# Optimization experiments

Hardware: AMD Instinct MI355X
Metric: run time of the kernel (lower is better)

The kernel has to match this reference:

```python
import jax, jax.numpy as jnp
import numpy as np
from jax import lax

SCALE = 0.05  # keep gates out of saturation

def _lstm_layer(x, w_ih, w_hh, b_ih, b_hh):
    # x: [B, T, In]; w_ih: [4H, In]; w_hh: [4H, H]; PyTorch gate order i,f,g,o
    B = x.shape[0]
    H = w_hh.shape[1]
    # precompute input contribution for all timesteps: [B, T, 4H]
    xg = jnp.einsum('bti,gi->btg', x, w_ih) + b_ih + b_hh
    h0 = jnp.zeros((B, H), dtype=x.dtype)
    c0 = jnp.zeros((B, H), dtype=x.dtype)

    def step(carry, xg_t):
        h, c = carry
        gates = xg_t + h @ w_hh.T  # [B, 4H]
        i, f, g, o = jnp.split(gates, 4, axis=-1)
        i = jax.nn.sigmoid(i)
        f = jax.nn.sigmoid(f)
        g = jnp.tanh(g)
        o = jax.nn.sigmoid(o)
        c = f * c + i * g
        h = o * jnp.tanh(c)
        return (h, c), h

    (h_T, c_T), hs = lax.scan(step, (h0, c0), xg.transpose(1, 0, 2))  # hs: [T, B, H]
    return hs.transpose(1, 0, 2), h_T, c_T


def setup_inputs() -> dict:
    key = jax.random.key(0)
    ks = jax.random.split(key, 12)
    B, T, In, H = 128, 1024, 128, 256
    G = 4 * H
    inp = {
        'x': jax.random.normal(ks[0], (B, T, In), dtype=jnp.float32),
        'w_ih_l0': jax.random.normal(ks[1], (G, In), dtype=jnp.float32) * SCALE,
        'w_hh_l0': jax.random.normal(ks[2], (G, H), dtype=jnp.float32) * SCALE,
        'b_ih_l0': jax.random.normal(ks[3], (G,), dtype=jnp.float32) * SCALE,
        'b_hh_l0': jax.random.normal(ks[4], (G,), dtype=jnp.float32) * SCALE,
        'w_ih_l1': jax.random.normal(ks[5], (G, H), dtype=jnp.float32) * SCALE,
        'w_hh_l1': jax.random.normal(ks[6], (G, H), dtype=jnp.float32) * SCALE,
        'b_ih_l1': jax.random.normal(ks[7], (G,), dtype=jnp.float32) * SCALE,
        'b_hh_l1': jax.random.normal(ks[8], (G,), dtype=jnp.float32) * SCALE,
        'w_lin': jax.random.normal(ks[9], (In, H), dtype=jnp.float32) * SCALE,
        'b_lin': jax.random.normal(ks[10], (In,), dtype=jnp.float32) * SCALE,
    }
    return inp


def reference(x, w_ih_l0, w_hh_l0, b_ih_l0, b_hh_l0,
              w_ih_l1, w_hh_l1, b_ih_l1, b_hh_l1, w_lin, b_lin):
    h0_seq, h0, c0 = _lstm_layer(x, w_ih_l0, w_hh_l0, b_ih_l0, b_hh_l0)
    h1_seq, h1, c1 = _lstm_layer(h0_seq, w_ih_l1, w_hh_l1, b_ih_l1, b_hh_l1)
    out = jnp.einsum('bth,oh->bto', h1_seq, w_lin) + b_lin  # [B, T, In]
    h = jnp.stack([h0, h1], axis=0)  # [num_layers, B, H]
    c = jnp.stack([c0, c1], axis=0)
    return out, (h, c)
```

## Files before the change

### kernel.cpp

```cpp
#include <hip/hip_runtime.h>
#include <hip/hip_bf16.h>

typedef __attribute__((ext_vector_type(8))) short short8;
typedef __attribute__((ext_vector_type(4))) float floatx4;
typedef __attribute__((ext_vector_type(4))) unsigned int uint4v;
typedef __attribute__((ext_vector_type(2))) _Float16 f16x2;

#define B_ 128
#define T_ 1024
#define H_ 256
#define G_ 1024

#if defined(__has_builtin)
#  if __has_builtin(__builtin_amdgcn_fdot2)
#    define HAS_FDOT2 1
#  endif
#endif

__device__ __forceinline__ float sigmoidf_(float x) {
    return 1.0f / (1.0f + __expf(-x));
}
__device__ __forceinline__ float tanhf_(float x) {
    float e = __expf(2.0f * x);
    return 1.0f - 2.0f / (e + 1.0f);
}
__device__ __forceinline__ unsigned short f2bu(float x) {
    __hip_bfloat16 b = __float2bfloat16(x);
    return *reinterpret_cast<unsigned short*>(&b);
}

__device__ __forceinline__ float dot2_(unsigned int w, unsigned int h, float acc) {
#ifdef HAS_FDOT2
    return __builtin_amdgcn_fdot2(__builtin_bit_cast(f16x2, w),
                                  __builtin_bit_cast(f16x2, h), acc, false);
#else
    float d;
    asm("v_dot2_f32_f16 %0, %1, %2, %3" : "=v"(d) : "v"(w), "v"(h), "v"(acc));
    return d;
#endif
}

struct GParam {
    const float* A;
    const float* Wt;
    const float* bias1;
    const float* bias2;
    float* C;
    int d2shift;
    long sa1, sa2, sc1, sc2;
    int K;
    int valid;
};

__global__ __launch_bounds__(256) void gemm_bias_f32(GParam P)
{
    __shared__ __hip_bfloat16 a_tile[64][40];
    __shared__ __hip_bfloat16 b_tile[64][40];

    const int tid  = threadIdx.x;
    const int wave = tid >> 6;
    const int lane = tid & 63;
    const int quad = lane >> 4;
    const int l16  = lane & 15;

    const int bm = blockIdx.x * 64;
    const int bn = blockIdx.y * 64;
    const int mask = (1 << P.d2shift) - 1;

    const int lr  = tid >> 2;
    const int seg = tid & 3;

    const int grow = bm + lr;
    const float* abase =
        P.A + (long)(grow >> P.d2shift) * P.sa1 + (long)(grow & mask) * P.sa2 + seg * 8;
    const float* bbase = P.Wt + (long)(bn + lr) * P.K + seg * 8;

    floatx4 acc[4];
    #pragma unroll
    for (int nt = 0; nt < 4; ++nt) acc[nt] = (floatx4){0.f, 0.f, 0.f, 0.f};

    for (int kk = 0; kk < P.K; kk += 32) {
        float4 a0 = *(const float4*)(abase + kk);
        float4 a1 = *(const float4*)(abase + kk + 4);
        float4 b0 = *(const float4*)(bbase + kk);
        float4 b1 = *(const float4*)(bbase + kk + 4);
        uint4 ap, bp;
        ap.x = f2bu(a0.x) | ((unsigned)f2bu(a0.y) << 16);
        ap.y = f2bu(a0.z) | ((unsigned)f2bu(a0.w) << 16);
        ap.z = f2bu(a1.x) | ((unsigned)f2bu(a1.y) << 16);
        ap.w = f2bu(a1.z) | ((unsigned)f2bu(a1.w) << 16);
        bp.x = f2bu(b0.x) | ((unsigned)f2bu(b0.y) << 16);
        bp.y = f2bu(b0.z) | ((unsigned)f2bu(b0.w) << 16);
        bp.z = f2bu(b1.x) | ((unsigned)f2bu(b1.y) << 16);
        bp.w = f2bu(b1.z) | ((unsigned)f2bu(b1.w) << 16);
        __syncthreads();
        *(uint4*)&a_tile[lr][seg * 8] = ap;
        *(uint4*)&b_tile[lr][seg * 8] = bp;
        __syncthreads();
        short8 af = *(const short8*)&a_tile[wave * 16 + l16][quad * 8];
        #pragma unroll
        for (int nt = 0; nt < 4; ++nt) {
            short8 bf = *(const short8*)&b_tile[nt * 16 + l16][quad * 8];
            acc[nt] = __builtin_amdgcn_mfma_f32_16x16x32_bf16(af, bf, acc[nt], 0, 0, 0);
        }
    }

    #pragma unroll
    for (int nt = 0; nt < 4; ++nt) {
        const int col = bn + nt * 16 + l16;
        float bsum = P.bias1[col];
        if (P.bias2) bsum += P.bias2[col];
        #pragma unroll
        for (int r = 0; r < 4; ++r) {
            const int rm = bm + wave * 16 + quad * 4 + r;
            const long off = (long)(rm >> P.d2shift) * P.sc1 + (long)(rm & mask) * P.sc2;
            P.C[off + col] = acc[nt][r] + bsum;
        }
    }
}

__global__ __launch_bounds__(256) void pack_whh(
    const float* __restrict__ w,
    unsigned int* __restrict__ wrg,
    unsigned int* __restrict__ wo)
{
    const int idx = blockIdx.x * 256 + threadIdx.x;
    if (idx < 98304) {
        const int kh = idx / 49152;
        const int r  = idx % 49152;
        const int g  = r >> 14;
        const int r2 = r & 16383;
        const int kp = r2 >> 8;
        const int jj = r2 & 255;
        const long src = (long)(g * 256 + jj) * 256 + kh * 128 + kp * 2;
        f16x2 pk;
        pk.x = (_Float16)w[src];
        pk.y = (_Float16)w[src + 1];
        wrg[idx] = __builtin_bit_cast(unsigned int, pk);
    } else {
        const int i2 = idx - 98304;
        const int jj = i2 >> 7;
        const int kp = i2 & 127;
        const long src = (long)(768 + jj) * 256 + kp * 2;
        f16x2 pk;
        pk.x = (_Float16)w[src];
        pk.y = (_Float16)w[src + 1];
        wo[i2] = __builtin_bit_cast(unsigned int, pk);
    }
}

struct LArgs {
    const float* xg;
    const unsigned int* wrg;
    const unsigned int* wo;
    float* h_seq;
    const float* h_in;
    const float* c_in;
    float* h_out;
    float* c_out;
    float* c_fin;
    int Tc;
    int init;
    int valid;
};

__device__ __forceinline__ void lstm_body(const LArgs& A, int b)
{
    const int tid = threadIdx.x;
    const int j   = tid & 255;
    const int kh  = tid >> 8;

    __shared__ __align__(16) unsigned int wo_lds[32768];
    __shared__ __align__(16) float part[256][4];
    __shared__ __align__(16) _Float16 hpk[256];

    const int Tc = A.Tc;

    unsigned int wi_[64], wf_[64], wg_[64];
    {
        const unsigned int* wb = A.wrg + (long)kh * 49152 + j;
        #pragma unroll
        for (int kp = 0; kp < 64; ++kp) wi_[kp] = wb[kp * 256];
        #pragma unroll
        for (int kp = 0; kp < 64; ++kp) wf_[kp] = wb[16384 + kp * 256];
        #pragma unroll
        for (int kp = 0; kp < 64; ++kp) wg_[kp] = wb[32768 + kp * 256];
    }

    for (int it = 0; it < 64; ++it) {
        const int d    = it * 512 + tid;
        const int jr   = d >> 7;
        const int kp   = d & 127;
        const int slot = (kp >> 2) ^ (jr & 31);
        wo_lds[jr * 128 + slot * 4 + (kp & 3)] = A.wo[d];
    }

    float c = 0.f, hlast = 0.f;
    if (kh == 0) {
        float h0 = 0.f;
        if (!A.init) {
            h0 = A.h_in[(long)b * H_ + j];
            c  = A.c_in[(long)b * H_ + j];
        }
        hlast = h0;
        hpk[j] = (_Float16)h0;
    }
    __syncthreads();

    const float* xbase = A.xg + (long)b * G_ + j;
    float nI = 0.f, nF = 0.f, nG = 0.f, nO = 0.f;
    if (kh == 0) {
        nI = xbase[0]; nF = xbase[256]; nG = xbase[512]; nO = xbase[768];
    }

    const int jx = j & 31;

    for (int t = 0; t < Tc; ++t) {
        __syncthreads();

        float aI = nI, aF = nF, aG = nG, aO = nO;
        if (kh == 0 && t + 1 < Tc) {
            const float* xn = xbase + (long)(t + 1) * (B_ * G_);
            nI = xn[0]; nF = xn[256]; nG = xn[512]; nO = xn[768];
        }

        #pragma unroll
        for (int q = 0; q < 16; ++q) {
            const int gi = kh * 16 + q;
            uint4v hv = *(const uint4v*)&hpk[gi * 8];
            uint4v wv = *(const uint4v*)&wo_lds[j * 128 + ((gi ^ jx) << 2)];
            #pragma unroll
            for (int e = 0; e < 4; ++e) {
                const int kp = q * 4 + e;
                aI = dot2_(wi_[kp], hv[e], aI);
                aF = dot2_(wf_[kp], hv[e], aF);
                aG = dot2_(wg_[kp], hv[e], aG);
                aO = dot2_(wv[e],   hv[e], aO);
            }
        }

        if (kh) {
            float4 pp; pp.x = aI; pp.y = aF; pp.z = aG; pp.w = aO;
            *(float4*)&part[j][0] = pp;
        }
        __syncthreads();
        if (!kh) {
            float4 pp = *(const float4*)&part[j][0];
            const float iv = sigmoidf_(aI + pp.x);
            const float fv = sigmoidf_(aF + pp.y);
            const float gv = tanhf_(aG + pp.z);
            const float ov = sigmoidf_(aO + pp.w);
            c = fv * c + iv * gv;
            const float hv2 = ov * tanhf_(c);
            hlast = hv2;
            A.h_seq[((long)t * B_ + b) * H_ + j] = hv2;
            hpk[j] = (_Float16)hv2;
        }
    }

    if (kh == 0) {
        A.h_out[(long)b * H_ + j] = hlast;
        A.c_out[(long)b * H_ + j] = c;
        if (A.c_fin) A.c_fin[(long)b * H_ + j] = c;
    }
}

__global__ __attribute__((amdgpu_waves_per_eu(2, 2)))
__launch_bounds__(512) void lstm_fused(LArgs a0, LArgs a1)
{
    const LArgs& A = (blockIdx.x < 128) ? a0 : a1;
    if (!A.valid) return;
    lstm_body(A, blockIdx.x & 127);
}

extern "C" void kernel_launch(void* const* d_in, const int* in_sizes, int n_in,
                              void* d_out, int out_size, void* d_ws, size_t ws_size,
                              hipStream_t stream)
{
    const float* x     = (const float*)d_in[0];
    const float* w_ih0 = (const float*)d_in[1];
    const float* w_hh0 = (const float*)d_in[2];
    const float* b_ih0 = (const float*)d_in[3];
    const float* b_hh0 = (const float*)d_in[4];
    const float* w_ih1 = (const float*)d_in[5];
    const float* w_hh1 = (const float*)d_in[6];
    const float* b_ih1 = (const float*)d_in[7];
    const float* b_hh1 = (const float*)d_in[8];
    const float* w_lin = (const float*)d_in[9];
    const float* b_lin = (const float*)d_in[10];

    float* out  = (float*)d_out;
    float* hfin = out + (size_t)B_ * T_ * 128;
    float* cfin = hfin + 2 * (B_ * H_);

    char* p = (char*)d_ws;
    unsigned int* wp0 = (unsigned int*)p;  p += 131072 * 4;
    unsigned int* wp1 = (unsigned int*)p;  p += 131072 * 4;
    float* h0st = (float*)p;  p += 131072;
    float* h1st = (float*)p;  p += 131072;
    float* c0st = (float*)p;  p += 131072;
    float* c1st = (float*)p;  p += 131072;
    const size_t fixed = (size_t)(p - (char*)d_ws);

    int Tc = 1024;
    while (Tc > 1 && fixed + (size_t)Tc * 1310720u > ws_size) Tc >>= 1;
    const int nc = T_ / Tc;
    const int tshift = __builtin_ctz((unsigned)Tc);

    float* xg0 = (float*)p;  p += (size_t)Tc * 524288;
    float* xg1 = (float*)p;  p += (size_t)Tc * 524288;
    float* h0c = (float*)p;  p += (size_t)Tc * 131072;
    float* h1c = (float*)p;

    pack_whh<<<dim3(512), dim3(256), 0, stream>>>(w_hh0, wp0, wp0 + 98304);
    pack_whh<<<dim3(512), dim3(256), 0, stream>>>(w_hh1, wp1, wp1 + 98304);

    LArgs inv{};  inv.valid = 0;

    auto L0args = [&](int i) {
        LArgs a;
        a.xg = xg0; a.wrg = wp0; a.wo = wp0 + 98304;
        a.h_seq = h0c; a.h_in = h0st; a.c_in = c0st;
        a.h_out = (i == nc - 1) ? hfin : h0st;
        a.c_out = c0st;
        a.c_fin = (i == nc - 1) ? cfin : (float*)nullptr;
        a.Tc = Tc; a.init = (i == 0); a.valid = 1;
        return a;
    };
    auto L1args = [&](int i) {
        LArgs a;
        a.xg = xg1; a.wrg = wp1; a.wo = wp1 + 98304;
        a.h_seq = h1c; a.h_in = h1st; a.c_in = c1st;
        a.h_out = (i == nc - 1) ? (hfin + B_ * H_) : h1st;
        a.c_out = c1st;
        a.c_fin = (i == nc - 1) ? (cfin + B_ * H_) : (float*)nullptr;
        a.Tc = Tc; a.init = (i == 0); a.valid = 1;
        return a;
    };

    auto Pg0 = [&](int i) {
        GParam P;
        P.A = x + (long)i * Tc * 128; P.Wt = w_ih0; P.bias1 = b_ih0; P.bias2 = b_hh0;
        P.C = xg0; P.d2shift = 7;
        P.sa1 = 128L; P.sa2 = 131072L; P.sc1 = 131072L; P.sc2 = 1024L;
        P.K = 128; P.valid = 1;
        return P;
    };
    auto Pg1 = [&](int i) {
        GParam P;
        P.A = h0c; P.Wt = w_ih1; P.bias1 = b_ih1; P.bias2 = b_hh1;
        P.C = xg1; P.d2shift = 7;
        P.sa1 = 32768L; P.sa2 = 256L; P.sc1 = 131072L; P.sc2 = 1024L;
        P.K = 256; P.valid = 1;
        return P;
    };
    auto Pout = [&](int i) {
        GParam P;
        P.A = h1c; P.Wt = w_lin; P.bias1 = b_lin; P.bias2 = nullptr;
        P.C = out + (long)i * Tc * 128; P.d2shift = tshift;
        P.sa1 = 256L; P.sa2 = 32768L; P.sc1 = 131072L; P.sc2 = 128L;
        P.K = 256; P.valid = 1;
        return P;
    };

    gemm_bias_f32<<<dim3(2 * Tc, 16), dim3(256), 0, stream>>>(Pg0(0));
    lstm_fused<<<dim3(256), dim3(512), 0, stream>>>(inv, L0args(0));

    for (int i = 0; i < nc; ++i) {
        gemm_bias_f32<<<dim3(2 * Tc, 16), dim3(256), 0, stream>>>(Pg1(i));

        if (i + 1 < nc)
            gemm_bias_f32<<<dim3(2 * Tc, 16), dim3(256), 0, stream>>>(Pg0(i + 1));

        lstm_fused<<<dim3(256), dim3(512), 0, stream>>>(
            L1args(i), (i + 1 < nc) ? L0args(i + 1) : inv);

        gemm_bias_f32<<<dim3(2 * Tc, 2), dim3(256), 0, stream>>>(Pout(i));
    }
}
```

Before: 2.401 ms.

## Pair K-halves in adjacent lanes, reduce with DPP, double-buffer hidden state

The two K-halves of each hidden unit's dot product move from threads 256 apart to adjacent lanes of the same wave. Their partial gate sums are combined with a DPP lane swap instead of an LDS partial buffer and an extra barrier. The hidden-state buffer is double-buffered, so each recurrent step needs one __syncthreads instead of two. In exchange both lanes compute the gate nonlinearities redundantly, and the one-time register weight loads become less coalesced.

```diff
diff --git a/kernel.cpp b/kernel.cpp
--- a/kernel.cpp
+++ b/kernel.cpp
@@ -38,6 +38,12 @@
     asm("v_dot2_f32_f16 %0, %1, %2, %3" : "=v"(d) : "v"(w), "v"(h), "v"(acc));
     return d;
 #endif
+}
+
+__device__ __forceinline__ float psum_(float x) {
+    int a = __builtin_bit_cast(int, x);
+    int b = __builtin_amdgcn_mov_dpp(a, 0xB1, 0xf, 0xf, true);
+    return x + __builtin_bit_cast(float, b);
 }
 
 struct GParam {
@@ -167,18 +173,17 @@
 __device__ __forceinline__ void lstm_body(const LArgs& A, int b)
 {
     const int tid = threadIdx.x;
-    const int j   = tid & 255;
-    const int kh  = tid >> 8;
+    const int j   = tid >> 1;
+    const int kq  = tid & 1;
 
     __shared__ __align__(16) unsigned int wo_lds[32768];
-    __shared__ __align__(16) float part[256][4];
-    __shared__ __align__(16) _Float16 hpk[256];
+    __shared__ __align__(16) _Float16 hpk[2][256];
 
     const int Tc = A.Tc;
 
     unsigned int wi_[64], wf_[64], wg_[64];
     {
-        const unsigned int* wb = A.wrg + (long)kh * 49152 + j;
+        const unsigned int* wb = A.wrg + (long)kq * 49152 + j;
         #pragma unroll
         for (int kp = 0; kp < 64; ++kp) wi_[kp] = wb[kp * 256];
         #pragma unroll
@@ -196,39 +201,36 @@
     }
 
     float c = 0.f, hlast = 0.f;
-    if (kh == 0) {
-        float h0 = 0.f;
-        if (!A.init) {
-            h0 = A.h_in[(long)b * H_ + j];
-            c  = A.c_in[(long)b * H_ + j];
-        }
+    if (!A.init) c = A.c_in[(long)b * H_ + j];
+    {
+        float h0 = A.init ? 0.f : A.h_in[(long)b * H_ + j];
         hlast = h0;
-        hpk[j] = (_Float16)h0;
+        if (kq == 0) hpk[0][j] = (_Float16)h0;
     }
     __syncthreads();
 
     const float* xbase = A.xg + (long)b * G_ + j;
     float nI = 0.f, nF = 0.f, nG = 0.f, nO = 0.f;
-    if (kh == 0) {
+    if (kq == 0) {
         nI = xbase[0]; nF = xbase[256]; nG = xbase[512]; nO = xbase[768];
     }
 
     const int jx = j & 31;
+    const unsigned int* worow = wo_lds + j * 128;
 
     for (int t = 0; t < Tc; ++t) {
-        __syncthreads();
-
         float aI = nI, aF = nF, aG = nG, aO = nO;
-        if (kh == 0 && t + 1 < Tc) {
+        if (kq == 0 && t + 1 < Tc) {
             const float* xn = xbase + (long)(t + 1) * (B_ * G_);
             nI = xn[0]; nF = xn[256]; nG = xn[512]; nO = xn[768];
         }
 
+        const _Float16* hb = &hpk[t & 1][0];
         #pragma unroll
         for (int q = 0; q < 16; ++q) {
-            const int gi = kh * 16 + q;
-            uint4v hv = *(const uint4v*)&hpk[gi * 8];
-            uint4v wv = *(const uint4v*)&wo_lds[j * 128 + ((gi ^ jx) << 2)];
+            const int gi = kq * 16 + q;
+            uint4v hv = *(const uint4v*)(hb + gi * 8);
+            uint4v wv = *(const uint4v*)(worow + ((gi ^ jx) << 2));
             #pragma unroll
             for (int e = 0; e < 4; ++e) {
                 const int kp = q * 4 + e;
@@ -239,34 +241,30 @@
             }
         }
 
-        if (kh) {
-            float4 pp; pp.x = aI; pp.y = aF; pp.z = aG; pp.w = aO;
-            *(float4*)&part[j][0] = pp;
+        aI = psum_(aI); aF = psum_(aF); aG = psum_(aG); aO = psum_(aO);
+
+        const float iv = sigmoidf_(aI);
+        const float fv = sigmoidf_(aF);
+        const float gv = tanhf_(aG);
+        const float ov = sigmoidf_(aO);
+        c = fv * c + iv * gv;
+        const float hv2 = ov * tanhf_(c);
+        hlast = hv2;
+        if (kq == 0) {
+            A.h_seq[((long)t * B_ + b) * H_ + j] = hv2;
+            hpk[(t + 1) & 1][j] = (_Float16)hv2;
         }
         __syncthreads();
-        if (!kh) {
-            float4 pp = *(const float4*)&part[j][0];
-            const float iv = sigmoidf_(aI + pp.x);
-            const float fv = sigmoidf_(aF + pp.y);
-            const float gv = tanhf_(aG + pp.z);
-            const float ov = sigmoidf_(aO + pp.w);
-            c = fv * c + iv * gv;
-            const float hv2 = ov * tanhf_(c);
-            hlast = hv2;
-            A.h_seq[((long)t * B_ + b) * H_ + j] = hv2;
-            hpk[j] = (_Float16)hv2;
-        }
-    }
-
-    if (kh == 0) {
+    }
+
+    if (kq == 0) {
         A.h_out[(long)b * H_ + j] = hlast;
         A.c_out[(long)b * H_ + j] = c;
         if (A.c_fin) A.c_fin[(long)b * H_ + j] = c;
     }
 }
 
-__global__ __attribute__((amdgpu_waves_per_eu(2, 2)))
-__launch_bounds__(512) void lstm_fused(LArgs a0, LArgs a1)
+__global__ __launch_bounds__(512, 2) void lstm_fused(LArgs a0, LArgs a1)
 {
     const LArgs& A = (blockIdx.x < 128) ? a0 : a1;
     if (!A.valid) return;
```

New measurement: 2.607 ms. +8.6%, slower.
